# Kernel tuning notes

Hardware: AMD Instinct MI355X
Metric: run time of the kernel (lower is better)

The kernel has to match this reference:

```python
import math
import jax, jax.numpy as jnp
import numpy as np

B, S, D = 16, 2048, 256

def setup_inputs() -> dict:
    key = jax.random.key(0)
    kq, kk, kv, km = jax.random.split(key, 4)
    q = jax.random.normal(kq, (B, S, D), dtype=jnp.float32)
    k = jax.random.normal(kk, (B, S, D), dtype=jnp.float32)
    v = jax.random.normal(kv, (B, S, D), dtype=jnp.float32)
    mask = jax.random.randint(km, (B, S, S), 0, 2, dtype=jnp.int32)
    return {"q": q, "k": k, "v": v, "mask": mask}

def reference(q, k, v, mask):
    dim_input = q.shape[-1]
    # scores: [B, S, S]
    scores = jnp.einsum('bqd,bkd->bqk', q, k) / math.sqrt(dim_input)
    # non-standard masking: masked positions set to 0.0 (NOT -inf) before softmax
    scores = jnp.where(mask == 0, jnp.float32(0.0), scores)
    att = jax.nn.softmax(scores, axis=-1)
    # original: if mask.sum() == 0, attention is all zeros
    att = jnp.where(mask.sum() > 0, att, jnp.zeros_like(att))
    return jnp.einsum('bqk,bkd->bqd', att, v)
```

## Files before the change

### kernel.cpp

```cpp
#include <hip/hip_runtime.h>


#define B_  16
#define S_  2048
#define D_  256
#define NT_ 64
#define TILE_BYTES 16384

typedef short bf16x8 __attribute__((ext_vector_type(8)));
typedef float f32x4  __attribute__((ext_vector_type(4)));

__device__ __forceinline__ unsigned short f2bf(float x) {
    union { float f; unsigned u; } c; c.f = x;
    unsigned u = c.u;
    u += 0x7FFFu + ((u >> 16) & 1u);
    return (unsigned short)(u >> 16);
}

#define GLDS(g, l) __builtin_amdgcn_global_load_lds( \
    (const __attribute__((address_space(1))) void*)(g), \
    (__attribute__((address_space(3))) void*)(l), 16, 0, 0)

#define WAITVM(N) asm volatile("s_waitcnt vmcnt(" #N ")" ::: "memory")
#define SCHEDB()  __builtin_amdgcn_sched_barrier(0)

__global__ __launch_bounds__(256)
void prep_all(const float* __restrict__ k, const float* __restrict__ v,
              char* __restrict__ kbf, char* __restrict__ vtbf)
{
    const int bid = blockIdx.x;
    if (bid < 4096) {
        const int gid = bid * 256 + threadIdx.x;
        const int d8  = gid & 31;
        const int kv  = (gid >> 5) & 2047;
        const int b   = gid >> 16;
        const float* src = k + (((size_t)(b * S_ + kv)) << 8) + d8 * 8;
        const float4 f0 = *(const float4*)src;
        const float4 f1 = *(const float4*)(src + 4);
        bf16x8 h;
        h[0] = (short)f2bf(f0.x); h[1] = (short)f2bf(f0.y);
        h[2] = (short)f2bf(f0.z); h[3] = (short)f2bf(f0.w);
        h[4] = (short)f2bf(f1.x); h[5] = (short)f2bf(f1.y);
        h[6] = (short)f2bf(f1.z); h[7] = (short)f2bf(f1.w);
        const int tile = kv >> 5, kvl = kv & 31;
        char* dst = kbf + (((size_t)(b * NT_ + tile)) << 14)
                        + (kvl << 9) + ((d8 * 16) ^ ((kvl & 7) << 4));
        *(bf16x8*)dst = h;
    } else {
        const int gid  = (bid - 4096) * 256 + threadIdx.x;
        const int d    = gid & 255;
        const int g    = (gid >> 8) & 3;
        const int tile = (gid >> 10) & 63;
        const int b    = gid >> 16;
        const int kv0  = tile * 32 + g * 8;
        const float* src = v + (((size_t)(b * S_ + kv0)) << 8) + d;
        bf16x8 h;
        #pragma unroll
        for (int j = 0; j < 8; ++j) h[j] = (short)f2bf(src[(size_t)j << 8]);
        char* dst = vtbf + (((size_t)(b * NT_ + tile)) << 14)
                         + (d << 6) + ((g * 16) ^ (((d >> 1) & 3) << 4));
        *(bf16x8*)dst = h;
    }
}

__global__ __launch_bounds__(256, 1)
void attn_main(const float* __restrict__ q, const int* __restrict__ mask,
               const char* __restrict__ kbf, const char* __restrict__ vtbf,
               float* __restrict__ out)
{
    __shared__ alignas(128) char lds[155648];

    const int tid  = threadIdx.x;
    const int wid  = tid >> 6;
    const int lane = tid & 63;
    const int ln15 = lane & 15;
    const int quad = lane >> 4;
    const int swzK = (ln15 & 7) << 4;
    const int swzA = ((ln15 >> 1) & 3) << 4;

    const int bid = blockIdx.x;
    const int bx  = (bid & 7) * 32 + (bid >> 3);
    const int b   = bx >> 4;
    const int qt  = bx & 15;
    const int qw  = qt * 128 + wid * 32;

    const float QS = 0.09016844f;
    bf16x8 aq[2][8];
    #pragma unroll
    for (int s = 0; s < 2; ++s) {
        const float* qrow = q + ((size_t)(b * S_ + qw + s * 16 + ln15)) * D_;
        #pragma unroll
        for (int ks = 0; ks < 8; ++ks) {
            const float4 f0 = *(const float4*)(qrow + ks * 32 + quad * 8);
            const float4 f1 = *(const float4*)(qrow + ks * 32 + quad * 8 + 4);
            bf16x8 a;
            a[0] = (short)f2bf(f0.x * QS); a[1] = (short)f2bf(f0.y * QS);
            a[2] = (short)f2bf(f0.z * QS); a[3] = (short)f2bf(f0.w * QS);
            a[4] = (short)f2bf(f1.x * QS); a[5] = (short)f2bf(f1.y * QS);
            a[6] = (short)f2bf(f1.z * QS); a[7] = (short)f2bf(f1.w * QS);
            aq[s][ks] = a;
        }
    }
    SCHEDB();

    bf16x8 ones;
    #pragma unroll
    for (int e = 0; e < 8; ++e) ones[e] = (short)0x3F80;

    f32x4 oacc[2][16];
    #pragma unroll
    for (int s = 0; s < 2; ++s)
        #pragma unroll
        for (int i = 0; i < 16; ++i) oacc[s][i] = (f32x4){0.f, 0.f, 0.f, 0.f};
    f32x4 lacc[2];
    lacc[0] = (f32x4){0.f, 0.f, 0.f, 0.f};
    lacc[1] = (f32x4){0.f, 0.f, 0.f, 0.f};

    const char* ktile = kbf  + (((size_t)b * NT_) << 14);
    const char* vtile = vtbf + (((size_t)b * NT_) << 14);
    const char* mrow0 = (const char*)(mask + ((size_t)(b * S_ + qt * 128)) * S_);
    char* pw = lds + 147456 + wid * 2048;
    const int cc = wid * 4;
    const int mlrow = (lane >> 3);
    const int mlcol = (lane & 7) * 16;

    const int mro = (wid * 32 + 4 * quad) * 128 + ln15 * 4;

    #pragma unroll
    for (int t = 0; t < 2; ++t) {
        #pragma unroll
        for (int c = 0; c < 4; ++c) {
            GLDS(ktile + t * 16384 + (cc + c) * 1024 + lane * 16,
                 lds +         t * 16384 + (cc + c) * 1024);
            GLDS(vtile + t * 16384 + (cc + c) * 1024 + lane * 16,
                 lds + 49152 + t * 16384 + (cc + c) * 1024);
        }
        #pragma unroll
        for (int c = 0; c < 4; ++c) {
            const int ch = cc + c;
            GLDS(mrow0 + (size_t)(ch * 8 + mlrow) * (S_ * 4) + t * 128 + mlcol,
                 lds + 98304 + t * 16384 + ch * 1024 + lane * 16);
        }
    }
    SCHEDB();

#define PHASE(T, CUR, BN, CNT)                                                  \
    {                                                                           \
        WAITVM(CNT);                                                            \
        SCHEDB();                                                               \
        __builtin_amdgcn_s_barrier();                                           \
        SCHEDB();                                                               \
        if ((T) + 2 < NT_) {                                                    \
            const int tn = (T) + 2;                                             \
            const char* kg_ = ktile + ((size_t)tn << 14);                       \
            const char* vg_ = vtile + ((size_t)tn << 14);                       \
            _Pragma("unroll")                                                   \
            for (int c = 0; c < 4; ++c) {                                       \
                GLDS(kg_ + (cc + c) * 1024 + lane * 16,                         \
                     lds + (BN) * 16384 +         (cc + c) * 1024);             \
                GLDS(vg_ + (cc + c) * 1024 + lane * 16,                         \
                     lds + 49152 + (BN) * 16384 + (cc + c) * 1024);             \
            }                                                                   \
            _Pragma("unroll")                                                   \
            for (int c = 0; c < 4; ++c) {                                       \
                const int ch = cc + c;                                          \
                GLDS(mrow0 + (size_t)(ch * 8 + mlrow) * (S_ * 4) + tn * 128 + mlcol, \
                     lds + 98304 + (BN) * 16384 + ch * 1024 + lane * 16);       \
            }                                                                   \
            SCHEDB();                                                           \
        }                                                                       \
        const char* kl = lds + (CUR) * 16384;                                   \
        const char* ml = lds + 98304 + (CUR) * 16384;                           \
        f32x4 sacc[2][2];                                                       \
        sacc[0][0] = (f32x4){0.f, 0.f, 0.f, 0.f};                               \
        sacc[0][1] = (f32x4){0.f, 0.f, 0.f, 0.f};                               \
        sacc[1][0] = (f32x4){0.f, 0.f, 0.f, 0.f};                               \
        sacc[1][1] = (f32x4){0.f, 0.f, 0.f, 0.f};                               \
        _Pragma("unroll")                                                       \
        for (int ks = 0; ks < 8; ++ks) {                                        \
            _Pragma("unroll")                                                   \
            for (int nt = 0; nt < 2; ++nt) {                                    \
                const int off = ((nt * 16 + ln15) << 9)                         \
                              + (((ks << 6) + (quad << 4)) ^ swzK);             \
                const bf16x8 bk = *(const bf16x8*)(kl + off);                   \
                sacc[0][nt] = __builtin_amdgcn_mfma_f32_16x16x32_bf16(aq[0][ks], bk, sacc[0][nt], 0, 0, 0); \
                sacc[1][nt] = __builtin_amdgcn_mfma_f32_16x16x32_bf16(aq[1][ks], bk, sacc[1][nt], 0, 0, 0); \
            }                                                                   \
        }                                                                       \
        _Pragma("unroll")                                                       \
        for (int s = 0; s < 2; ++s) {                                           \
            _Pragma("unroll")                                                   \
            for (int nt = 0; nt < 2; ++nt) {                                    \
                _Pragma("unroll")                                               \
                for (int r = 0; r < 4; ++r) {                                   \
                    const int mv = *(const int*)(ml + mro + (s * 16 + r) * 128 + nt * 64); \
                    const float p = (mv != 0) ? exp2f(sacc[s][nt][r]) : 1.0f;   \
                    const int row  = s * 16 + 4 * quad + r;                     \
                    const int boff = (row << 6)                                 \
                                   + ((nt * 32 + ln15 * 2) ^ (((row >> 1) & 3) << 4)); \
                    *(unsigned short*)(pw + boff) = f2bf(p);                    \
                }                                                               \
            }                                                                   \
        }                                                                       \
        const bf16x8 ap0 = *(const bf16x8*)(pw + (ln15 << 6)        + ((quad << 4) ^ swzA)); \
        const bf16x8 ap1 = *(const bf16x8*)(pw + ((16 + ln15) << 6) + ((quad << 4) ^ swzA)); \
        const char* vl = lds + 49152 + (CUR) * 16384;                           \
        lacc[0] = __builtin_amdgcn_mfma_f32_16x16x32_bf16(ap0, ones, lacc[0], 0, 0, 0); \
        lacc[1] = __builtin_amdgcn_mfma_f32_16x16x32_bf16(ap1, ones, lacc[1], 0, 0, 0); \
        _Pragma("unroll")                                                       \
        for (int nt2 = 0; nt2 < 16; ++nt2) {                                    \
            const int voff = ((nt2 * 16 + ln15) << 6) + ((quad << 4) ^ swzA);   \
            const bf16x8 bv = *(const bf16x8*)(vl + voff);                      \
            oacc[0][nt2] = __builtin_amdgcn_mfma_f32_16x16x32_bf16(ap0, bv, oacc[0][nt2], 0, 0, 0); \
            oacc[1][nt2] = __builtin_amdgcn_mfma_f32_16x16x32_bf16(ap1, bv, oacc[1][nt2], 0, 0, 0); \
        }                                                                       \
        SCHEDB();                                                               \
    }

    for (int t3 = 0; t3 < 21; ++t3) {
        const int t = t3 * 3;
        PHASE(t + 0, 0, 2, 12);
        PHASE(t + 1, 1, 0, 12);
        PHASE(t + 2, 2, 1, 12);
    }
    PHASE(63, 0, 2, 0);
#undef PHASE

    #pragma unroll
    for (int s = 0; s < 2; ++s) {
        #pragma unroll
        for (int r = 0; r < 4; ++r) {
            const float inv = 1.0f / lacc[s][r];
            float* orow = out + ((size_t)(b * S_ + qw + s * 16 + 4 * quad + r)) * D_ + ln15;
            #pragma unroll
            for (int nt2 = 0; nt2 < 16; ++nt2)
                orow[nt2 * 16] = oacc[s][nt2][r] * inv;
        }
    }
}

#define QT 128
#define KTF 64
#define NW 8
#define KSTR 264
#define VSTR 72
#define PSTR 72

__global__ __launch_bounds__(512, 2)
void attn_fused_v1(const float* __restrict__ q, const float* __restrict__ k,
                   const float* __restrict__ v, const int* __restrict__ mask,
                   float* __restrict__ out)
{
    __shared__ unsigned short Kl[KTF * KSTR];
    __shared__ unsigned short Vt[D_ * VSTR];
    __shared__ unsigned short Pl[NW][16 * PSTR];

    const int tid  = threadIdx.x;
    const int wid  = tid >> 6;
    const int lane = tid & 63;
    const int ln15 = lane & 15;
    const int quad = lane >> 4;
    const int bid = blockIdx.x;
    const int bx  = (bid & 7) * 32 + (bid >> 3);
    const int b  = bx >> 4;
    const int qt = bx & 15;
    const int qw = qt * QT + wid * 16;

    const float* qb = q + ((size_t)b * S_ + qw) * D_;
    const float* kb = k + (size_t)b * S_ * D_;
    const float* vb = v + (size_t)b * S_ * D_;
    const int*   mb = mask + ((size_t)b * S_ + qw) * (size_t)S_;

    bf16x8 aq[8];
    {
        const float* qrow = qb + (size_t)ln15 * D_;
        #pragma unroll
        for (int ks = 0; ks < 8; ++ks) {
            const float4 f0 = *(const float4*)(qrow + ks * 32 + quad * 8);
            const float4 f1 = *(const float4*)(qrow + ks * 32 + quad * 8 + 4);
            bf16x8 a;
            a[0] = (short)f2bf(f0.x * 0.0625f); a[1] = (short)f2bf(f0.y * 0.0625f);
            a[2] = (short)f2bf(f0.z * 0.0625f); a[3] = (short)f2bf(f0.w * 0.0625f);
            a[4] = (short)f2bf(f1.x * 0.0625f); a[5] = (short)f2bf(f1.y * 0.0625f);
            a[6] = (short)f2bf(f1.z * 0.0625f); a[7] = (short)f2bf(f1.w * 0.0625f);
            aq[ks] = a;
        }
    }
    bf16x8 ones;
    #pragma unroll
    for (int e = 0; e < 8; ++e) ones[e] = (short)0x3F80;
    f32x4 oacc[16];
    #pragma unroll
    for (int i = 0; i < 16; ++i) oacc[i] = (f32x4){0.f, 0.f, 0.f, 0.f};
    f32x4 lacc = (f32x4){0.f, 0.f, 0.f, 0.f};
    const int kst_c0 = (tid & 63) * 4;

    for (int kt2 = 0; kt2 < S_ / KTF; ++kt2) {
        const int kvbase = kt2 * KTF;
        int mval[4][4];
        #pragma unroll
        for (int nt = 0; nt < 4; ++nt)
            #pragma unroll
            for (int r = 0; r < 4; ++r)
                mval[nt][r] = mb[(size_t)(4 * quad + r) * S_ + kvbase + nt * 16 + ln15];
        __syncthreads();
        {
            const float* ks_ = kb + (size_t)kvbase * D_;
            #pragma unroll
            for (int pass = 0; pass < 8; ++pass) {
                const int r = pass * 8 + wid;
                const float4 f = *(const float4*)(ks_ + (size_t)r * D_ + kst_c0);
                ushort4 hh;
                hh.x = f2bf(f.x); hh.y = f2bf(f.y); hh.z = f2bf(f.z); hh.w = f2bf(f.w);
                *(ushort4*)&Kl[r * KSTR + kst_c0] = hh;
            }
        }
        {
            const float* vs_ = vb + (size_t)kvbase * D_;
            #pragma unroll
            for (int pass = 0; pass < 8; ++pass) {
                const int idx = pass * 8 + wid;
                const int kv  = (idx & 3) * 16 + ln15;
                const int d0  = (idx >> 2) * 16 + 4 * quad;
                const float4 f = *(const float4*)(vs_ + (size_t)kv * D_ + d0);
                Vt[(d0 + 0) * VSTR + kv] = f2bf(f.x);
                Vt[(d0 + 1) * VSTR + kv] = f2bf(f.y);
                Vt[(d0 + 2) * VSTR + kv] = f2bf(f.z);
                Vt[(d0 + 3) * VSTR + kv] = f2bf(f.w);
            }
        }
        __syncthreads();
        f32x4 sacc[4];
        #pragma unroll
        for (int nt = 0; nt < 4; ++nt) sacc[nt] = (f32x4){0.f, 0.f, 0.f, 0.f};
        #pragma unroll
        for (int ks = 0; ks < 8; ++ks) {
            #pragma unroll
            for (int nt = 0; nt < 4; ++nt) {
                const bf16x8 bk =
                    *(const bf16x8*)&Kl[(nt * 16 + ln15) * KSTR + ks * 32 + quad * 8];
                sacc[nt] = __builtin_amdgcn_mfma_f32_16x16x32_bf16(aq[ks], bk, sacc[nt], 0, 0, 0);
            }
        }
        unsigned short* pwv = Pl[wid];
        #pragma unroll
        for (int nt = 0; nt < 4; ++nt) {
            #pragma unroll
            for (int r = 0; r < 4; ++r) {
                const float s = sacc[nt][r];
                const float p = (mval[nt][r] != 0) ? __expf(s) : 1.0f;
                pwv[(4 * quad + r) * PSTR + nt * 16 + ln15] = f2bf(p);
            }
        }
        #pragma unroll
        for (int ks2 = 0; ks2 < 2; ++ks2) {
            const bf16x8 ap = *(const bf16x8*)&pwv[ln15 * PSTR + ks2 * 32 + quad * 8];
            lacc = __builtin_amdgcn_mfma_f32_16x16x32_bf16(ap, ones, lacc, 0, 0, 0);
            #pragma unroll
            for (int nt2 = 0; nt2 < 16; ++nt2) {
                const bf16x8 bv =
                    *(const bf16x8*)&Vt[(nt2 * 16 + ln15) * VSTR + ks2 * 32 + quad * 8];
                oacc[nt2] = __builtin_amdgcn_mfma_f32_16x16x32_bf16(ap, bv, oacc[nt2], 0, 0, 0);
            }
        }
    }
    #pragma unroll
    for (int r = 0; r < 4; ++r) {
        const float inv = 1.0f / lacc[r];
        float* orow = out + ((size_t)b * S_ + qw + 4 * quad + r) * D_ + ln15;
        #pragma unroll
        for (int nt2 = 0; nt2 < 16; ++nt2)
            orow[nt2 * 16] = oacc[nt2][r] * inv;
    }
}

extern "C" void kernel_launch(void* const* d_in, const int* in_sizes, int n_in,
                              void* d_out, int out_size, void* d_ws, size_t ws_size,
                              hipStream_t stream) {
    const float* q    = (const float*)d_in[0];
    const float* k    = (const float*)d_in[1];
    const float* v    = (const float*)d_in[2];
    const int*   mask = (const int*)d_in[3];
    float*       out  = (float*)d_out;

    const size_t one = (size_t)B_ * NT_ * TILE_BYTES;
    if (ws_size >= 2 * one) {
        char* kbf  = (char*)d_ws;
        char* vtbf = kbf + one;
        prep_all<<<8192, 256, 0, stream>>>(k, v, kbf, vtbf);
        attn_main<<<256, 256, 0, stream>>>(q, mask, kbf, vtbf, out);
    } else {
        attn_fused_v1<<<256, 512, 0, stream>>>(q, k, v, mask, out);
    }
}
```

Before: 162.1 us.

## Prefetch mask into registers and pack into per-wave bitmasks in LDS

```diff
diff --git a/kernel.cpp b/kernel.cpp
--- a/kernel.cpp
+++ b/kernel.cpp
@@ -68,7 +68,7 @@
                const char* __restrict__ kbf, const char* __restrict__ vtbf,
                float* __restrict__ out)
 {
-    __shared__ alignas(128) char lds[155648];
+    __shared__ alignas(128) char lds[124928];
 
     const int tid  = threadIdx.x;
     const int wid  = tid >> 6;
@@ -77,6 +77,7 @@
     const int quad = lane >> 4;
     const int swzK = (ln15 & 7) << 4;
     const int swzA = ((ln15 >> 1) & 3) << 4;
+    const int mshift = ((ln15 >> 2) << 3) + (ln15 & 3);
 
     const int bid = blockIdx.x;
     const int bx  = (bid & 7) * 32 + (bid >> 3);
@@ -118,16 +119,15 @@
 
     const char* ktile = kbf  + (((size_t)b * NT_) << 14);
     const char* vtile = vtbf + (((size_t)b * NT_) << 14);
-    const char* mrow0 = (const char*)(mask + ((size_t)(b * S_ + qt * 128)) * S_);
-    char* pw = lds + 147456 + wid * 2048;
+    char* pw  = lds + 98304 + wid * 2048;
+    char* pmw = lds + 106496 + wid * 4608;
     const int cc = wid * 4;
-    const int mlrow = (lane >> 3);
-    const int mlcol = (lane & 7) * 16;
-
-    const int mro = (wid * 32 + 4 * quad) * 128 + ln15 * 4;
-
-    #pragma unroll
-    for (int t = 0; t < 2; ++t) {
+
+    const char* mbase8 = (const char*)mask + ((size_t)(b * S_ + qw)) * (S_ * 4);
+    int4 mp[4];
+
+    #pragma unroll
+    for (int t = 0; t < 2; ++t)
         #pragma unroll
         for (int c = 0; c < 4; ++c) {
             GLDS(ktile + t * 16384 + (cc + c) * 1024 + lane * 16,
@@ -135,11 +135,28 @@
             GLDS(vtile + t * 16384 + (cc + c) * 1024 + lane * 16,
                  lds + 49152 + t * 16384 + (cc + c) * 1024);
         }
-        #pragma unroll
-        for (int c = 0; c < 4; ++c) {
-            const int ch = cc + c;
-            GLDS(mrow0 + (size_t)(ch * 8 + mlrow) * (S_ * 4) + t * 128 + mlcol,
-                 lds + 98304 + t * 16384 + ch * 1024 + lane * 16);
+    SCHEDB();
+    {
+        int4 pa[4], pb[4];
+        #pragma unroll
+        for (int r4 = 0; r4 < 4; ++r4)
+            pa[r4] = *(const int4*)(mbase8 + (size_t)r4 * 8192 + (size_t)(4 * lane) * 4);
+        #pragma unroll
+        for (int j = 0; j < 8; ++j) {
+            if (j < 7)
+                #pragma unroll
+                for (int r4 = 0; r4 < 4; ++r4)
+                    pb[r4] = *(const int4*)(mbase8 + (size_t)(4 * (j + 1) + r4) * 8192
+                                            + (size_t)(4 * lane) * 4);
+            #pragma unroll
+            for (int r4 = 0; r4 < 4; ++r4) {
+                const int4 m = pa[r4];
+                const unsigned nib = (m.x != 0 ? 1u : 0u) | (m.y != 0 ? 2u : 0u)
+                                   | (m.z != 0 ? 4u : 0u) | (m.w != 0 ? 8u : 0u);
+                pmw[(4 * j + r4) * 72 + lane] = (unsigned char)nib;
+            }
+            #pragma unroll
+            for (int r4 = 0; r4 < 4; ++r4) pa[r4] = pb[r4];
         }
     }
     SCHEDB();
@@ -150,8 +167,9 @@
         SCHEDB();                                                               \
         __builtin_amdgcn_s_barrier();                                           \
         SCHEDB();                                                               \
-        if ((T) + 2 < NT_) {                                                    \
-            const int tn = (T) + 2;                                             \
+        const int T_ = (T);                                                     \
+        if (T_ <= 61) {                                                         \
+            const int tn = T_ + 2;                                              \
             const char* kg_ = ktile + ((size_t)tn << 14);                       \
             const char* vg_ = vtile + ((size_t)tn << 14);                       \
             _Pragma("unroll")                                                   \
@@ -161,16 +179,9 @@
                 GLDS(vg_ + (cc + c) * 1024 + lane * 16,                         \
                      lds + 49152 + (BN) * 16384 + (cc + c) * 1024);             \
             }                                                                   \
-            _Pragma("unroll")                                                   \
-            for (int c = 0; c < 4; ++c) {                                       \
-                const int ch = cc + c;                                          \
-                GLDS(mrow0 + (size_t)(ch * 8 + mlrow) * (S_ * 4) + tn * 128 + mlcol, \
-                     lds + 98304 + (BN) * 16384 + ch * 1024 + lane * 16);       \
-            }                                                                   \
             SCHEDB();                                                           \
         }                                                                       \
         const char* kl = lds + (CUR) * 16384;                                   \
-        const char* ml = lds + 98304 + (CUR) * 16384;                           \
         f32x4 sacc[2][2];                                                       \
         sacc[0][0] = (f32x4){0.f, 0.f, 0.f, 0.f};                               \
         sacc[0][1] = (f32x4){0.f, 0.f, 0.f, 0.f};                               \
@@ -187,15 +198,31 @@
                 sacc[1][nt] = __builtin_amdgcn_mfma_f32_16x16x32_bf16(aq[1][ks], bk, sacc[1][nt], 0, 0, 0); \
             }                                                                   \
         }                                                                       \
+        SCHEDB();                                                               \
+        if (T_ >= 1 && T_ <= 56) {             \
+            char* pmpk = pmw + ((((((T_) - 1) >> 3) + 1) & 1) ? 2304 : 0);      \
+            const int rb = 4 * (((T_) - 1) & 7);                                \
+            _Pragma("unroll")                                                   \
+            for (int r4 = 0; r4 < 4; ++r4) {                                    \
+                const int4 m = mp[r4];                                          \
+                const unsigned nib = (m.x != 0 ? 1u : 0u) | (m.y != 0 ? 2u : 0u)\
+                                   | (m.z != 0 ? 4u : 0u) | (m.w != 0 ? 8u : 0u);\
+                pmpk[(rb + r4) * 72 + lane] = (unsigned char)nib;               \
+            }                                                                   \
+        }                                                                       \
+        SCHEDB();                                                               \
+        const char* pmr = pmw + ((((T_) >> 3) & 1) ? 2304 : 0) + 8 * ((T_) & 7);\
         _Pragma("unroll")                                                       \
         for (int s = 0; s < 2; ++s) {                                           \
             _Pragma("unroll")                                                   \
-            for (int nt = 0; nt < 2; ++nt) {                                    \
+            for (int r = 0; r < 4; ++r) {                                       \
+                const int row = s * 16 + 4 * quad + r;                          \
+                const unsigned long long wb = *(const unsigned long long*)(pmr + row * 72); \
+                const unsigned wlo = (unsigned)wb, whi = (unsigned)(wb >> 32);  \
                 _Pragma("unroll")                                               \
-                for (int r = 0; r < 4; ++r) {                                   \
-                    const int mv = *(const int*)(ml + mro + (s * 16 + r) * 128 + nt * 64); \
-                    const float p = (mv != 0) ? exp2f(sacc[s][nt][r]) : 1.0f;   \
-                    const int row  = s * 16 + 4 * quad + r;                     \
+                for (int nt = 0; nt < 2; ++nt) {                                \
+                    const unsigned bit = ((nt ? whi : wlo) >> mshift) & 1u;     \
+                    const float p = bit ? exp2f(sacc[s][nt][r]) : 1.0f;         \
                     const int boff = (row << 6)                                 \
                                    + ((nt * 32 + ln15 * 2) ^ (((row >> 1) & 3) << 4)); \
                     *(unsigned short*)(pw + boff) = f2bf(p);                    \
@@ -215,14 +242,28 @@
             oacc[1][nt2] = __builtin_amdgcn_mfma_f32_16x16x32_bf16(ap1, bv, oacc[1][nt2], 0, 0, 0); \
         }                                                                       \
         SCHEDB();                                                               \
-    }
-
-    for (int t3 = 0; t3 < 21; ++t3) {
+        if (T_ <= 55) {              \
+            const int rb2 = 4 * ((T_) & 7);                                     \
+            const size_t c0b = (size_t)((((T_) >> 3) + 1) * 256 + 4 * lane) * 4;\
+            _Pragma("unroll")                                                   \
+            for (int r4 = 0; r4 < 4; ++r4)                                      \
+                mp[r4] = *(const int4*)(mbase8 + (size_t)(rb2 + r4) * 8192 + c0b); \
+        }                                                                       \
+        SCHEDB();                                                               \
+    }
+
+    for (int t3 = 0; t3 < 19; ++t3) {
         const int t = t3 * 3;
         PHASE(t + 0, 0, 2, 12);
         PHASE(t + 1, 1, 0, 12);
         PHASE(t + 2, 2, 1, 12);
     }
+    PHASE(57, 0, 2, 8);
+    PHASE(58, 1, 0, 8);
+    PHASE(59, 2, 1, 8);
+    PHASE(60, 0, 2, 8);
+    PHASE(61, 1, 0, 8);
+    PHASE(62, 2, 1, 8);
     PHASE(63, 0, 2, 0);
 #undef PHASE
 
```

Measured after the change: 188.1 us. +16.0%, slower.

## Pre-pack int32 mask rows into LDS bitmasks before the main attention loop

Applied to the files above, without the earlier changes.

```diff
diff --git a/kernel.cpp b/kernel.cpp
--- a/kernel.cpp
+++ b/kernel.cpp
@@ -68,7 +68,7 @@
                const char* __restrict__ kbf, const char* __restrict__ vtbf,
                float* __restrict__ out)
 {
-    __shared__ alignas(128) char lds[155648];
+    __shared__ alignas(128) char lds[139264];
 
     const int tid  = threadIdx.x;
     const int wid  = tid >> 6;
@@ -103,31 +103,14 @@
     }
     SCHEDB();
 
-    bf16x8 ones;
-    #pragma unroll
-    for (int e = 0; e < 8; ++e) ones[e] = (short)0x3F80;
-
-    f32x4 oacc[2][16];
-    #pragma unroll
-    for (int s = 0; s < 2; ++s)
-        #pragma unroll
-        for (int i = 0; i < 16; ++i) oacc[s][i] = (f32x4){0.f, 0.f, 0.f, 0.f};
-    f32x4 lacc[2];
-    lacc[0] = (f32x4){0.f, 0.f, 0.f, 0.f};
-    lacc[1] = (f32x4){0.f, 0.f, 0.f, 0.f};
-
     const char* ktile = kbf  + (((size_t)b * NT_) << 14);
     const char* vtile = vtbf + (((size_t)b * NT_) << 14);
-    const char* mrow0 = (const char*)(mask + ((size_t)(b * S_ + qt * 128)) * S_);
-    char* pw = lds + 147456 + wid * 2048;
+    char* pw = lds + 98304 + wid * 2048;
+    unsigned* pmL = (unsigned*)(lds + 106496);
     const int cc = wid * 4;
-    const int mlrow = (lane >> 3);
-    const int mlcol = (lane & 7) * 16;
-
-    const int mro = (wid * 32 + 4 * quad) * 128 + ln15 * 4;
-
-    #pragma unroll
-    for (int t = 0; t < 2; ++t) {
+
+    #pragma unroll
+    for (int t = 0; t < 2; ++t)
         #pragma unroll
         for (int c = 0; c < 4; ++c) {
             GLDS(ktile + t * 16384 + (cc + c) * 1024 + lane * 16,
@@ -135,14 +118,48 @@
             GLDS(vtile + t * 16384 + (cc + c) * 1024 + lane * 16,
                  lds + 49152 + t * 16384 + (cc + c) * 1024);
         }
-        #pragma unroll
-        for (int c = 0; c < 4; ++c) {
-            const int ch = cc + c;
-            GLDS(mrow0 + (size_t)(ch * 8 + mlrow) * (S_ * 4) + t * 128 + mlcol,
-                 lds + 98304 + t * 16384 + ch * 1024 + lane * 16);
-        }
-    }
     SCHEDB();
+
+    {
+        char* scratch = lds + 98304 + wid * 512;
+        const char* mrow = (const char*)mask + ((size_t)(b * S_) + qw) * 8192;
+        for (int r = 0; r < 32; ++r) {
+            const char* src = mrow + (size_t)r * 8192 + lane * 16;
+            int4 m[8];
+            #pragma unroll
+            for (int j = 0; j < 8; ++j)
+                m[j] = *(const int4*)(src + j * 1024);
+            #pragma unroll
+            for (int j = 0; j < 8; ++j) {
+                const unsigned nib = (unsigned)(m[j].x != 0)
+                                   | ((unsigned)(m[j].y != 0) << 1)
+                                   | ((unsigned)(m[j].z != 0) << 2)
+                                   | ((unsigned)(m[j].w != 0) << 3);
+                scratch[j * 64 + lane] = (char)nib;
+            }
+            const unsigned long long u =
+                *(const unsigned long long*)(scratch + lane * 8);
+            unsigned w = 0;
+            #pragma unroll
+            for (int i = 0; i < 8; ++i)
+                w |= ((unsigned)(u >> (8 * i)) & 0xFu) << (4 * i);
+            pmL[(wid * 32 + r) * 64 + lane] = w;
+        }
+    }
+    SCHEDB();
+
+    bf16x8 ones;
+    #pragma unroll
+    for (int e = 0; e < 8; ++e) ones[e] = (short)0x3F80;
+
+    f32x4 oacc[2][16];
+    #pragma unroll
+    for (int s = 0; s < 2; ++s)
+        #pragma unroll
+        for (int i = 0; i < 16; ++i) oacc[s][i] = (f32x4){0.f, 0.f, 0.f, 0.f};
+    f32x4 lacc[2];
+    lacc[0] = (f32x4){0.f, 0.f, 0.f, 0.f};
+    lacc[1] = (f32x4){0.f, 0.f, 0.f, 0.f};
 
 #define PHASE(T, CUR, BN, CNT)                                                  \
     {                                                                           \
@@ -161,16 +178,9 @@
                 GLDS(vg_ + (cc + c) * 1024 + lane * 16,                         \
                      lds + 49152 + (BN) * 16384 + (cc + c) * 1024);             \
             }                                                                   \
-            _Pragma("unroll")                                                   \
-            for (int c = 0; c < 4; ++c) {                                       \
-                const int ch = cc + c;                                          \
-                GLDS(mrow0 + (size_t)(ch * 8 + mlrow) * (S_ * 4) + tn * 128 + mlcol, \
-                     lds + 98304 + (BN) * 16384 + ch * 1024 + lane * 16);       \
-            }                                                                   \
             SCHEDB();                                                           \
         }                                                                       \
         const char* kl = lds + (CUR) * 16384;                                   \
-        const char* ml = lds + 98304 + (CUR) * 16384;                           \
         f32x4 sacc[2][2];                                                       \
         sacc[0][0] = (f32x4){0.f, 0.f, 0.f, 0.f};                               \
         sacc[0][1] = (f32x4){0.f, 0.f, 0.f, 0.f};                               \
@@ -190,12 +200,13 @@
         _Pragma("unroll")                                                       \
         for (int s = 0; s < 2; ++s) {                                           \
             _Pragma("unroll")                                                   \
-            for (int nt = 0; nt < 2; ++nt) {                                    \
+            for (int r = 0; r < 4; ++r) {                                       \
+                const int row = s * 16 + 4 * quad + r;                          \
+                const unsigned w = pmL[(wid * 32 + row) * 64 + (T)];            \
                 _Pragma("unroll")                                               \
-                for (int r = 0; r < 4; ++r) {                                   \
-                    const int mv = *(const int*)(ml + mro + (s * 16 + r) * 128 + nt * 64); \
-                    const float p = (mv != 0) ? exp2f(sacc[s][nt][r]) : 1.0f;   \
-                    const int row  = s * 16 + 4 * quad + r;                     \
+                for (int nt = 0; nt < 2; ++nt) {                                \
+                    const float p = ((w >> (nt * 16 + ln15)) & 1u)              \
+                                  ? exp2f(sacc[s][nt][r]) : 1.0f;               \
                     const int boff = (row << 6)                                 \
                                    + ((nt * 32 + ln15 * 2) ^ (((row >> 1) & 3) << 4)); \
                     *(unsigned short*)(pw + boff) = f2bf(p);                    \
@@ -214,14 +225,13 @@
             oacc[0][nt2] = __builtin_amdgcn_mfma_f32_16x16x32_bf16(ap0, bv, oacc[0][nt2], 0, 0, 0); \
             oacc[1][nt2] = __builtin_amdgcn_mfma_f32_16x16x32_bf16(ap1, bv, oacc[1][nt2], 0, 0, 0); \
         }                                                                       \
-        SCHEDB();                                                               \
     }
 
     for (int t3 = 0; t3 < 21; ++t3) {
         const int t = t3 * 3;
-        PHASE(t + 0, 0, 2, 12);
-        PHASE(t + 1, 1, 0, 12);
-        PHASE(t + 2, 2, 1, 12);
+        PHASE(t + 0, 0, 2, 8);
+        PHASE(t + 1, 1, 0, 8);
+        PHASE(t + 2, 2, 1, 8);
     }
     PHASE(63, 0, 2, 0);
 #undef PHASE
```

Measured after the change: 204.7 us. 26.2% more time.
